# Performance work log

Hardware: AMD Instinct MI355X
Metric: run time of the kernel (lower is better)

Reference implementation:

```python
import jax, jax.numpy as jnp
import numpy as np

ALPHA = 0.2  # LeakyReLU negative slope
NEG_INF = -9e15


def setup_inputs() -> dict:
    key = jax.random.key(0)
    k1, k2, k3, k4, k5 = jax.random.split(key, 5)
    B, N, D = 4, 4096, 256
    feat = jax.random.normal(k1, (B, N, D), dtype=jnp.float32)
    adj = jax.random.randint(k2, (B, N, N), 0, 2, dtype=jnp.int32)
    W = jax.random.normal(k3, (D, D), dtype=jnp.float32) * (1.414 / np.sqrt(D))
    a_1 = jax.random.normal(k4, (D, 1), dtype=jnp.float32) * 0.1
    a_2 = jax.random.normal(k5, (D, 1), dtype=jnp.float32) * 0.1
    return {"feat": feat, "adj": adj, "W": W, "a_1": a_1, "a_2": a_2}


def reference(feat, adj, W, a_1, a_2):
    # h: [B, N, D]
    h = jnp.matmul(feat, W)
    Ax = jnp.matmul(h, a_1)  # [B, N, 1]
    Ay = jnp.matmul(h, a_2)  # [B, N, 1]
    # logits[b, i, j] = Ax[b, j] + Ay[b, i]
    logits = jnp.swapaxes(Ax, 1, 2) + Ay  # [B, N, N]
    e = jax.nn.leaky_relu(logits, negative_slope=ALPHA)
    e = jnp.where(adj > 0, e, jnp.float32(NEG_INF))
    attention = jax.nn.softmax(e, axis=-1)  # dropout p=0.0 -> identity
    h_prime = jnp.matmul(attention, feat)  # [B, N, in_features]
    h_out = jnp.matmul(h_prime, W)  # [B, N, out_features]
    return jax.nn.elu(h_out)
```

## Files before the change

kernel.cpp:

```cpp
#include <hip/hip_runtime.h>

typedef __attribute__((ext_vector_type(8))) short short8;
typedef __attribute__((ext_vector_type(4))) float f32x4;
typedef __attribute__((ext_vector_type(4))) int i32x4;
typedef __attribute__((ext_vector_type(2))) unsigned u32x2;

#define LOG2E 1.44269504f

__device__ __forceinline__ short f2bf(float f) {
  unsigned u = __builtin_bit_cast(unsigned, f);
  u += 0x7fffu + ((u >> 16) & 1u);
  return (short)(u >> 16);
}

__global__ __launch_bounds__(256) void gat_pro(
    const float* __restrict__ feat, const float* __restrict__ W,
    const float* __restrict__ a1, const float* __restrict__ a2,
    short* __restrict__ featB, short* __restrict__ WB,
    float* __restrict__ AxL, float* __restrict__ AyL) {
  __shared__ __align__(16) float a1f[256], a2f[256];
  __shared__ __align__(16) float w1f[256], w2f[256];
  __shared__ __align__(16) float tile[32][260];
  const int tid = threadIdx.x;
  const int f = blockIdx.x, b = blockIdx.y;

  a1f[tid] = a1[tid];
  a2f[tid] = a2[tid];
  __syncthreads();

  {
    float s1 = 0.f, s2 = 0.f;
    const float4* wr = (const float4*)(W + (size_t)tid * 256);
    for (int d0 = 0; d0 < 64; ++d0) {
      float4 v = wr[d0];
      s1 += v.x * a1f[d0 * 4] + v.y * a1f[d0 * 4 + 1] + v.z * a1f[d0 * 4 + 2] + v.w * a1f[d0 * 4 + 3];
      s2 += v.x * a2f[d0 * 4] + v.y * a2f[d0 * 4 + 1] + v.z * a2f[d0 * 4 + 2] + v.w * a2f[d0 * 4 + 3];
    }
    w1f[tid] = s1;
    w2f[tid] = s2;
  }
  __syncthreads();

  {
    const int r = tid >> 3, g8 = tid & 7;
    const float* frow = feat + ((size_t)(b * 4096 + f * 32 + r)) * 256;
    float s1 = 0.f, s2 = 0.f;
#pragma unroll
    for (int k = 0; k < 8; ++k) {
      const int c4 = g8 + 8 * k;
      float4 v = *(const float4*)(frow + c4 * 4);
      float4 u1 = *(const float4*)&w1f[c4 * 4];
      float4 u2 = *(const float4*)&w2f[c4 * 4];
      s1 += v.x * u1.x + v.y * u1.y + v.z * u1.z + v.w * u1.w;
      s2 += v.x * u2.x + v.y * u2.y + v.z * u2.z + v.w * u2.w;
      *(float4*)&tile[r][c4 * 4] = v;
    }
#pragma unroll
    for (int off = 4; off >= 1; off >>= 1) {
      s1 += __shfl_xor(s1, off);
      s2 += __shfl_xor(s2, off);
    }
    if (g8 == 0) {
      AxL[b * 4096 + f * 32 + r] = s1 * LOG2E;
      AyL[b * 4096 + f * 32 + r] = s2 * LOG2E;
    }
  }
  __syncthreads();

  {
    const int g = tid >> 4, l15 = tid & 15;
    short* d = featB + (((size_t)((b * 128 + f) * 16 + g)) * 64) * 8;
#pragma unroll
    for (int q = 0; q < 4; ++q) {
      short8 v;
#pragma unroll
      for (int j8 = 0; j8 < 8; ++j8) v[j8] = f2bf(tile[q * 8 + j8][g * 16 + l15]);
      *(short8*)(d + (q * 16 + l15) * 8) = v;
    }
  }

  if (b == 0 && f < 8) {
    const int g = tid >> 4, l15 = tid & 15;
    const float* s = W + ((size_t)f * 32) * 256 + g * 16 + l15;
    short* d = WB + (((size_t)(f * 16 + g)) * 64) * 8;
#pragma unroll
    for (int q = 0; q < 4; ++q) {
      short8 v;
#pragma unroll
      for (int j8 = 0; j8 < 8; ++j8) v[j8] = f2bf(s[(q * 8 + j8) * 256]);
      *(short8*)(d + (q * 16 + l15) * 8) = v;
    }
  }
}

__global__ __launch_bounds__(512, 2) void gat_attn(
    const short* __restrict__ featB,
    const int* __restrict__ adj,
    const float* __restrict__ AxL, const float* __restrict__ AyL,
    const short* __restrict__ WB,
    float* __restrict__ out)
{
  __shared__ short smem[33792];
  __shared__ float mred[8];

  const int tid = threadIdx.x;
  const int blk = blockIdx.x;
  const int x = blk & 7;
  const int b = x >> 1;
  const int it = ((blk >> 3) << 1) | (x & 1);
  const int i0 = it << 6;
  const int scoff = (blk >> 3) & 15;

  const int lane = tid & 63;
  const int aw = tid >> 6;

  const float* axb = AxL + b * 4096;
  float mx = -3.4e38f;
  for (int i = tid; i < 4096; i += 512) mx = fmaxf(mx, axb[i]);
#pragma unroll
  for (int off = 32; off >= 1; off >>= 1) mx = fmaxf(mx, __shfl_xor(mx, off));
  if (lane == 0) mred[aw] = mx;
  __syncthreads();
  const float MbLb = fmaxf(fmaxf(fmaxf(mred[0], mred[1]), fmaxf(mred[2], mred[3])),
                           fmaxf(fmaxf(mred[4], mred[5]), fmaxf(mred[6], mred[7])));

  float aLk[8], ddk[8];
#pragma unroll
  for (int k = 0; k < 8; ++k) {
    float ayL = AyL[b * 4096 + i0 + aw * 8 + k];
    float sL = ayL + MbLb;
    float mrL = fmaxf(sL, 0.2f * sL);
    aLk[k] = ayL - mrL;
    ddk[k] = -0.8f * mrL;
  }
  const int* adjr = adj + ((size_t)(b * 4096 + i0 + aw * 8)) * 4096 + lane * 4;
  const float4* axp = (const float4*)(AxL + b * 4096) + lane;

  const int rowg = (aw & 1) << 4;
  const int cgrp = (aw >> 1) << 2;
  const int l15 = lane & 15;
  const int q = lane >> 4;

  f32x4 acc[2][4], lac[2];
#pragma unroll
  for (int r = 0; r < 2; ++r) {
    lac[r] = (f32x4){0.f, 0.f, 0.f, 0.f};
#pragma unroll
    for (int j = 0; j < 4; ++j) acc[r][j] = (f32x4){0.f, 0.f, 0.f, 0.f};
  }

  short8 ones;
#pragma unroll
  for (int j = 0; j < 8; ++j) ones[j] = (short)0x3F80;

  const short* fbb = featB + (size_t)b * 128 * 16 * 64 * 8 + lane * 8;

  i32x4 adv[8];
  float4 axv;
  {
    const int w0 = scoff;
    axv = axp[w0 * 64];
#pragma unroll
    for (int k = 0; k < 8; ++k)
      adv[k] = __builtin_nontemporal_load((const i32x4*)(adjr) + (size_t)k * 1024 + w0 * 64);
  }

  for (int sc = 0; sc < 16; ++sc) {
    const int wsc = (scoff + sc) & 15;
    const int pb = (sc & 1) * 16896;
    {
      const float* af = (const float*)&axv;
#pragma unroll
      for (int k = 0; k < 8; ++k) {
        unsigned pr[4];
#pragma unroll
        for (int u = 0; u < 4; ++u) {
          float v = af[u] + aLk[k];
          float uu = fmaxf(v, fmaf(0.2f, v, ddk[k]));
          unsigned ub = adv[k][u] > 0 ? __builtin_bit_cast(unsigned, uu) : 0xFF800000u;
          float p = __builtin_amdgcn_exp2f(__builtin_bit_cast(float, ub));
          pr[u] = __builtin_bit_cast(unsigned, p) + 0x8000u;
        }
        u32x2 pw;
        pw[0] = __builtin_amdgcn_perm(pr[1], pr[0], 0x07060302u);
        pw[1] = __builtin_amdgcn_perm(pr[3], pr[2], 0x07060302u);
        *(u32x2*)(smem + pb + (aw * 8 + k) * 264 + lane * 4) = pw;
      }
    }
    __syncthreads();

    if (sc < 15) {
      const int wn = (scoff + sc + 1) & 15;
      axv = axp[wn * 64];
#pragma unroll
      for (int k = 0; k < 8; ++k)
        adv[k] = __builtin_nontemporal_load((const i32x4*)(adjr) + (size_t)k * 1024 + wn * 64);
    }

#pragma unroll
    for (int h = 0; h < 8; ++h) {
      const int f = wsc * 8 + h;
      const short* fb = fbb + (((size_t)f * 16 + cgrp) << 9);
      short8 a0 = *(const short8*)(smem + pb + (rowg + l15) * 264 + h * 32 + q * 8);
      short8 a1 = *(const short8*)(smem + pb + (rowg + 32 + l15) * 264 + h * 32 + q * 8);
      lac[0] = __builtin_amdgcn_mfma_f32_16x16x32_bf16(a0, ones, lac[0], 0, 0, 0);
      lac[1] = __builtin_amdgcn_mfma_f32_16x16x32_bf16(a1, ones, lac[1], 0, 0, 0);
#pragma unroll
      for (int ct = 0; ct < 4; ++ct) {
        short8 bf = *(const short8*)(fb + (ct << 9));
        acc[0][ct] = __builtin_amdgcn_mfma_f32_16x16x32_bf16(a0, bf, acc[0][ct], 0, 0, 0);
        acc[1][ct] = __builtin_amdgcn_mfma_f32_16x16x32_bf16(a1, bf, acc[1][ct], 0, 0, 0);
      }
    }
  }

  float linv[2][4];
#pragma unroll
  for (int r = 0; r < 2; ++r)
#pragma unroll
    for (int reg = 0; reg < 4; ++reg) {
      float l = lac[r][reg];
      linv[r][reg] = l > 0.f ? 1.f / l : 0.f;
    }

  __syncthreads();
  short* hbuf = smem;
#pragma unroll
  for (int r = 0; r < 2; ++r)
#pragma unroll
    for (int reg = 0; reg < 4; ++reg) {
      const int lr = rowg + r * 32 + q * 4 + reg;
#pragma unroll
      for (int ct = 0; ct < 4; ++ct)
        hbuf[lr * 264 + cgrp * 16 + ct * 16 + l15] = f2bf(acc[r][ct][reg] * linv[r][reg]);
    }
  __syncthreads();

  f32x4 ac2[2][4];
#pragma unroll
  for (int r = 0; r < 2; ++r)
#pragma unroll
    for (int j = 0; j < 4; ++j) ac2[r][j] = (f32x4){0.f, 0.f, 0.f, 0.f};

  const short* wbb = WB + lane * 8;
#pragma unroll
  for (int f = 0; f < 8; ++f) {
    short8 a0 = *(const short8*)&hbuf[(rowg + l15) * 264 + f * 32 + q * 8];
    short8 a1 = *(const short8*)&hbuf[(rowg + 32 + l15) * 264 + f * 32 + q * 8];
    const short* wb = wbb + (((size_t)f * 16 + cgrp) << 9);
#pragma unroll
    for (int ct = 0; ct < 4; ++ct) {
      short8 bf = *(const short8*)(wb + (ct << 9));
      ac2[0][ct] = __builtin_amdgcn_mfma_f32_16x16x32_bf16(a0, bf, ac2[0][ct], 0, 0, 0);
      ac2[1][ct] = __builtin_amdgcn_mfma_f32_16x16x32_bf16(a1, bf, ac2[1][ct], 0, 0, 0);
    }
  }

#pragma unroll
  for (int r = 0; r < 2; ++r)
#pragma unroll
    for (int reg = 0; reg < 4; ++reg) {
      const int row = i0 + rowg + r * 32 + q * 4 + reg;
      float* orow = out + ((size_t)(b * 4096 + row)) * 256 + cgrp * 16 + l15;
#pragma unroll
      for (int ct = 0; ct < 4; ++ct) {
        float v = ac2[r][ct][reg];
        float o = v > 0.f ? v : (__builtin_amdgcn_exp2f(v * LOG2E) - 1.f);
        __builtin_nontemporal_store(o, orow + ct * 16);
      }
    }
}

extern "C" void kernel_launch(void* const* d_in, const int* in_sizes, int n_in,
                              void* d_out, int out_size, void* d_ws, size_t ws_size,
                              hipStream_t stream) {
  (void)in_sizes; (void)n_in; (void)out_size; (void)ws_size;
  const float* feat = (const float*)d_in[0];
  const int* adj = (const int*)d_in[1];
  const float* W = (const float*)d_in[2];
  const float* a1 = (const float*)d_in[3];
  const float* a2 = (const float*)d_in[4];
  float* out = (float*)d_out;

  char* ws = (char*)d_ws;
  short* featB   = (short*)ws;
  short* WB      = (short*)(ws + 8388608);
  float* AxL     = (float*)(ws + 8519680);
  float* AyL     = (float*)(ws + 8585216);

  hipLaunchKernelGGL(gat_pro, dim3(128, 4), dim3(256), 0, stream, feat, W, a1, a2, featB, WB, AxL, AyL);
  hipLaunchKernelGGL(gat_attn, dim3(256), dim3(512), 0, stream, featB, adj, AxL, AyL, WB, out);
}
```

Measured before the change: 429.1 us.

## Split main loop into producer and consumer waves for warp specialization

Splits the 8 waves into 4 producer waves and 4 consumer waves. Producers load adjacency, compute the masked exponentials and write bf16 probabilities into a double-buffered shared tile one chunk ahead. Consumers run all the MFMA work on 64 rows by 64 columns each. The aim is to overlap the exp/VALU work and global loads with the matrix multiplies. The cost is a higher per-wave register load (16 adjacency vectors, or 16 accumulators) and only half the waves issuing MFMA, so occupancy or MFMA throughput may suffer.

```diff
diff --git a/kernel.cpp b/kernel.cpp
--- a/kernel.cpp
+++ b/kernel.cpp
@@ -113,6 +113,8 @@
 
   const int lane = tid & 63;
   const int aw = tid >> 6;
+  const int l15 = lane & 15;
+  const int q = lane >> 4;
 
   const float* axb = AxL + b * 4096;
   float mx = -3.4e38f;
@@ -124,117 +126,129 @@
   const float MbLb = fmaxf(fmaxf(fmaxf(mred[0], mred[1]), fmaxf(mred[2], mred[3])),
                            fmaxf(fmaxf(mred[4], mred[5]), fmaxf(mred[6], mred[7])));
 
-  float aLk[8], ddk[8];
-#pragma unroll
-  for (int k = 0; k < 8; ++k) {
-    float ayL = AyL[b * 4096 + i0 + aw * 8 + k];
-    float sL = ayL + MbLb;
-    float mrL = fmaxf(sL, 0.2f * sL);
-    aLk[k] = ayL - mrL;
-    ddk[k] = -0.8f * mrL;
-  }
-  const int* adjr = adj + ((size_t)(b * 4096 + i0 + aw * 8)) * 4096 + lane * 4;
+  const bool producer = (aw < 4);
+
+  const int pw = aw & 3;
+  float aLk[16], ddk[16];
+  const int* adjr = adj + ((size_t)(b * 4096 + i0 + pw * 16)) * 4096 + lane * 4;
   const float4* axp = (const float4*)(AxL + b * 4096) + lane;
+  i32x4 adv[16];
+  float4 axv;
+
+  const int cg = (aw & 3) << 2;
+  const short* fbb = featB + (size_t)b * 128 * 16 * 64 * 8 + lane * 8;
+  f32x4 acc[4][4], lac[4];
+#pragma unroll
+  for (int r = 0; r < 4; ++r) {
+    lac[r] = (f32x4){0.f, 0.f, 0.f, 0.f};
+#pragma unroll
+    for (int j = 0; j < 4; ++j) acc[r][j] = (f32x4){0.f, 0.f, 0.f, 0.f};
+  }
+  short8 ones;
+#pragma unroll
+  for (int j = 0; j < 8; ++j) ones[j] = (short)0x3F80;
+
+  if (producer) {
+#pragma unroll
+    for (int k = 0; k < 16; ++k) {
+      float ayL = AyL[b * 4096 + i0 + pw * 16 + k];
+      float sL = ayL + MbLb;
+      float mrL = fmaxf(sL, 0.2f * sL);
+      aLk[k] = ayL - mrL;
+      ddk[k] = -0.8f * mrL;
+    }
+  }
+
+  auto computeP = [&](int bufSel) {
+    const float* af = (const float*)&axv;
+#pragma unroll
+    for (int k = 0; k < 16; ++k) {
+      unsigned pr[4];
+#pragma unroll
+      for (int u = 0; u < 4; ++u) {
+        float v = af[u] + aLk[k];
+        float uu = fmaxf(v, fmaf(0.2f, v, ddk[k]));
+        unsigned ub = adv[k][u] > 0 ? __builtin_bit_cast(unsigned, uu) : 0xFF800000u;
+        float p = __builtin_amdgcn_exp2f(__builtin_bit_cast(float, ub));
+        pr[u] = __builtin_bit_cast(unsigned, p) + 0x8000u;
+      }
+      u32x2 pw2;
+      pw2[0] = __builtin_amdgcn_perm(pr[1], pr[0], 0x07060302u);
+      pw2[1] = __builtin_amdgcn_perm(pr[3], pr[2], 0x07060302u);
+      *(u32x2*)(smem + bufSel * 16896 + (pw * 16 + k) * 264 + lane * 4) = pw2;
+    }
+  };
+  auto prefetchW = [&](int w) {
+    axv = axp[w * 64];
+#pragma unroll
+    for (int k = 0; k < 16; ++k)
+      adv[k] = __builtin_nontemporal_load((const i32x4*)(adjr) + (size_t)k * 1024 + w * 64);
+  };
+
+  if (producer) {
+    prefetchW(scoff);
+    computeP(0);
+    prefetchW((scoff + 1) & 15);
+  }
+  __syncthreads();
+
+  for (int sc = 0; sc < 16; ++sc) {
+    if (producer) {
+      if (sc < 15) {
+        computeP((sc + 1) & 1);
+        if (sc < 14) prefetchW((scoff + sc + 2) & 15);
+      }
+    } else {
+      const int wsc = (scoff + sc) & 15;
+      const int pb = (sc & 1) * 16896;
+#pragma unroll
+      for (int h = 0; h < 8; ++h) {
+        const int f = wsc * 8 + h;
+        const short* fb = fbb + (((size_t)f * 16 + cg) << 9);
+        short8 a[4];
+#pragma unroll
+        for (int r = 0; r < 4; ++r)
+          a[r] = *(const short8*)(smem + pb + (r * 16 + l15) * 264 + h * 32 + q * 8);
+#pragma unroll
+        for (int r = 0; r < 4; ++r)
+          lac[r] = __builtin_amdgcn_mfma_f32_16x16x32_bf16(a[r], ones, lac[r], 0, 0, 0);
+#pragma unroll
+        for (int ct = 0; ct < 4; ++ct) {
+          short8 bf = *(const short8*)(fb + (ct << 9));
+#pragma unroll
+          for (int r = 0; r < 4; ++r)
+            acc[r][ct] = __builtin_amdgcn_mfma_f32_16x16x32_bf16(a[r], bf, acc[r][ct], 0, 0, 0);
+        }
+      }
+    }
+    __syncthreads();
+  }
+
+  if (!producer) {
+    float linv[4][4];
+#pragma unroll
+    for (int r = 0; r < 4; ++r)
+#pragma unroll
+      for (int reg = 0; reg < 4; ++reg) {
+        float l = lac[r][reg];
+        linv[r][reg] = l > 0.f ? 1.f / l : 0.f;
+      }
+    short* hbuf = smem;
+#pragma unroll
+    for (int r = 0; r < 4; ++r)
+#pragma unroll
+      for (int reg = 0; reg < 4; ++reg) {
+        const int lr = r * 16 + q * 4 + reg;
+#pragma unroll
+        for (int ct = 0; ct < 4; ++ct)
+          hbuf[lr * 264 + (cg + ct) * 16 + l15] = f2bf(acc[r][ct][reg] * linv[r][reg]);
+      }
+  }
+  __syncthreads();
 
   const int rowg = (aw & 1) << 4;
   const int cgrp = (aw >> 1) << 2;
-  const int l15 = lane & 15;
-  const int q = lane >> 4;
-
-  f32x4 acc[2][4], lac[2];
-#pragma unroll
-  for (int r = 0; r < 2; ++r) {
-    lac[r] = (f32x4){0.f, 0.f, 0.f, 0.f};
-#pragma unroll
-    for (int j = 0; j < 4; ++j) acc[r][j] = (f32x4){0.f, 0.f, 0.f, 0.f};
-  }
-
-  short8 ones;
-#pragma unroll
-  for (int j = 0; j < 8; ++j) ones[j] = (short)0x3F80;
-
-  const short* fbb = featB + (size_t)b * 128 * 16 * 64 * 8 + lane * 8;
-
-  i32x4 adv[8];
-  float4 axv;
-  {
-    const int w0 = scoff;
-    axv = axp[w0 * 64];
-#pragma unroll
-    for (int k = 0; k < 8; ++k)
-      adv[k] = __builtin_nontemporal_load((const i32x4*)(adjr) + (size_t)k * 1024 + w0 * 64);
-  }
-
-  for (int sc = 0; sc < 16; ++sc) {
-    const int wsc = (scoff + sc) & 15;
-    const int pb = (sc & 1) * 16896;
-    {
-      const float* af = (const float*)&axv;
-#pragma unroll
-      for (int k = 0; k < 8; ++k) {
-        unsigned pr[4];
-#pragma unroll
-        for (int u = 0; u < 4; ++u) {
-          float v = af[u] + aLk[k];
-          float uu = fmaxf(v, fmaf(0.2f, v, ddk[k]));
-          unsigned ub = adv[k][u] > 0 ? __builtin_bit_cast(unsigned, uu) : 0xFF800000u;
-          float p = __builtin_amdgcn_exp2f(__builtin_bit_cast(float, ub));
-          pr[u] = __builtin_bit_cast(unsigned, p) + 0x8000u;
-        }
-        u32x2 pw;
-        pw[0] = __builtin_amdgcn_perm(pr[1], pr[0], 0x07060302u);
-        pw[1] = __builtin_amdgcn_perm(pr[3], pr[2], 0x07060302u);
-        *(u32x2*)(smem + pb + (aw * 8 + k) * 264 + lane * 4) = pw;
-      }
-    }
-    __syncthreads();
-
-    if (sc < 15) {
-      const int wn = (scoff + sc + 1) & 15;
-      axv = axp[wn * 64];
-#pragma unroll
-      for (int k = 0; k < 8; ++k)
-        adv[k] = __builtin_nontemporal_load((const i32x4*)(adjr) + (size_t)k * 1024 + wn * 64);
-    }
-
-#pragma unroll
-    for (int h = 0; h < 8; ++h) {
-      const int f = wsc * 8 + h;
-      const short* fb = fbb + (((size_t)f * 16 + cgrp) << 9);
-      short8 a0 = *(const short8*)(smem + pb + (rowg + l15) * 264 + h * 32 + q * 8);
-      short8 a1 = *(const short8*)(smem + pb + (rowg + 32 + l15) * 264 + h * 32 + q * 8);
-      lac[0] = __builtin_amdgcn_mfma_f32_16x16x32_bf16(a0, ones, lac[0], 0, 0, 0);
-      lac[1] = __builtin_amdgcn_mfma_f32_16x16x32_bf16(a1, ones, lac[1], 0, 0, 0);
-#pragma unroll
-      for (int ct = 0; ct < 4; ++ct) {
-        short8 bf = *(const short8*)(fb + (ct << 9));
-        acc[0][ct] = __builtin_amdgcn_mfma_f32_16x16x32_bf16(a0, bf, acc[0][ct], 0, 0, 0);
-        acc[1][ct] = __builtin_amdgcn_mfma_f32_16x16x32_bf16(a1, bf, acc[1][ct], 0, 0, 0);
-      }
-    }
-  }
-
-  float linv[2][4];
-#pragma unroll
-  for (int r = 0; r < 2; ++r)
-#pragma unroll
-    for (int reg = 0; reg < 4; ++reg) {
-      float l = lac[r][reg];
-      linv[r][reg] = l > 0.f ? 1.f / l : 0.f;
-    }
-
-  __syncthreads();
   short* hbuf = smem;
-#pragma unroll
-  for (int r = 0; r < 2; ++r)
-#pragma unroll
-    for (int reg = 0; reg < 4; ++reg) {
-      const int lr = rowg + r * 32 + q * 4 + reg;
-#pragma unroll
-      for (int ct = 0; ct < 4; ++ct)
-        hbuf[lr * 264 + cgrp * 16 + ct * 16 + l15] = f2bf(acc[r][ct][reg] * linv[r][reg]);
-    }
-  __syncthreads();
 
   f32x4 ac2[2][4];
 #pragma unroll
```

Result: slower. 441.7 us (+2.9%).

## Pack adjacency into bitmasks in prologue kernel and read bits in attention

Applied to the files above, without the earlier changes.

Adds a second z-slice to the prologue kernel that reads the int32 adjacency matrix and packs it into 64-bit ballot bitmasks in workspace. The attention kernel then loads one 64-bit word per row chunk instead of int32 vectors and tests bits to apply the mask. This shrinks adjacency traffic in the MFMA-heavy attention kernel, but the full 256 MB adjacency read still happens, now in the prologue, plus an extra small write and read. Overall bytes do not drop, so any benefit depends on moving that read out of the compute-overlapped loop.

```diff
diff --git a/kernel.cpp b/kernel.cpp
--- a/kernel.cpp
+++ b/kernel.cpp
@@ -2,8 +2,8 @@
 
 typedef __attribute__((ext_vector_type(8))) short short8;
 typedef __attribute__((ext_vector_type(4))) float f32x4;
-typedef __attribute__((ext_vector_type(4))) int i32x4;
 typedef __attribute__((ext_vector_type(2))) unsigned u32x2;
+typedef __attribute__((ext_vector_type(4))) unsigned long long ull4;
 
 #define LOG2E 1.44269504f
 
@@ -16,13 +16,38 @@
 __global__ __launch_bounds__(256) void gat_pro(
     const float* __restrict__ feat, const float* __restrict__ W,
     const float* __restrict__ a1, const float* __restrict__ a2,
+    const int* __restrict__ adj,
     short* __restrict__ featB, short* __restrict__ WB,
-    float* __restrict__ AxL, float* __restrict__ AyL) {
+    float* __restrict__ AxL, float* __restrict__ AyL,
+    unsigned long long* __restrict__ adjP) {
+  const int tid = threadIdx.x;
+  const int f = blockIdx.x, b = blockIdx.y;
+
+  if (blockIdx.z == 1) {
+    const int wv = tid >> 6, l = tid & 63;
+#pragma unroll 1
+    for (int r = 0; r < 8; ++r) {
+      const int row = f * 32 + wv * 8 + r;
+      const int* src = adj + ((size_t)(b * 4096 + row)) * 4096;
+      unsigned long long* dst = adjP + ((size_t)(b * 4096 + row)) * 64;
+#pragma unroll 4
+      for (int jc = 0; jc < 16; ++jc) {
+        unsigned long long m0 = __ballot(src[jc * 256 + 0 * 64 + l] > 0);
+        unsigned long long m1 = __ballot(src[jc * 256 + 1 * 64 + l] > 0);
+        unsigned long long m2 = __ballot(src[jc * 256 + 2 * 64 + l] > 0);
+        unsigned long long m3 = __ballot(src[jc * 256 + 3 * 64 + l] > 0);
+        if (l == 0) {
+          ull4 mv = (ull4){m0, m1, m2, m3};
+          *(ull4*)(dst + jc * 4) = mv;
+        }
+      }
+    }
+    return;
+  }
+
   __shared__ __align__(16) float a1f[256], a2f[256];
   __shared__ __align__(16) float w1f[256], w2f[256];
   __shared__ __align__(16) float tile[32][260];
-  const int tid = threadIdx.x;
-  const int f = blockIdx.x, b = blockIdx.y;
 
   a1f[tid] = a1[tid];
   a2f[tid] = a2[tid];
@@ -95,7 +120,7 @@
 
 __global__ __launch_bounds__(512, 2) void gat_attn(
     const short* __restrict__ featB,
-    const int* __restrict__ adj,
+    const unsigned long long* __restrict__ adjP,
     const float* __restrict__ AxL, const float* __restrict__ AyL,
     const short* __restrict__ WB,
     float* __restrict__ out)
@@ -133,8 +158,10 @@
     aLk[k] = ayL - mrL;
     ddk[k] = -0.8f * mrL;
   }
-  const int* adjr = adj + ((size_t)(b * 4096 + i0 + aw * 8)) * 4096 + lane * 4;
+  const unsigned long long* adjPr =
+      adjP + ((size_t)(b * 4096 + i0 + aw * 8)) * 64 + (lane >> 4);
   const float4* axp = (const float4*)(AxL + b * 4096) + lane;
+  const int sh = (lane & 15) * 4;
 
   const int rowg = (aw & 1) << 4;
   const int cgrp = (aw >> 1) << 2;
@@ -155,14 +182,13 @@
 
   const short* fbb = featB + (size_t)b * 128 * 16 * 64 * 8 + lane * 8;
 
-  i32x4 adv[8];
+  unsigned long long adv[8];
   float4 axv;
   {
     const int w0 = scoff;
     axv = axp[w0 * 64];
 #pragma unroll
-    for (int k = 0; k < 8; ++k)
-      adv[k] = __builtin_nontemporal_load((const i32x4*)(adjr) + (size_t)k * 1024 + w0 * 64);
+    for (int k = 0; k < 8; ++k) adv[k] = adjPr[(size_t)k * 64 + w0 * 4];
   }
 
   for (int sc = 0; sc < 16; ++sc) {
@@ -177,7 +203,8 @@
         for (int u = 0; u < 4; ++u) {
           float v = af[u] + aLk[k];
           float uu = fmaxf(v, fmaf(0.2f, v, ddk[k]));
-          unsigned ub = adv[k][u] > 0 ? __builtin_bit_cast(unsigned, uu) : 0xFF800000u;
+          unsigned ub = ((adv[k] >> (sh + u)) & 1ull)
+                            ? __builtin_bit_cast(unsigned, uu) : 0xFF800000u;
           float p = __builtin_amdgcn_exp2f(__builtin_bit_cast(float, ub));
           pr[u] = __builtin_bit_cast(unsigned, p) + 0x8000u;
         }
@@ -193,8 +220,7 @@
       const int wn = (scoff + sc + 1) & 15;
       axv = axp[wn * 64];
 #pragma unroll
-      for (int k = 0; k < 8; ++k)
-        adv[k] = __builtin_nontemporal_load((const i32x4*)(adjr) + (size_t)k * 1024 + wn * 64);
+      for (int k = 0; k < 8; ++k) adv[k] = adjPr[(size_t)k * 64 + wn * 4];
     }
 
 #pragma unroll
@@ -283,11 +309,14 @@
   float* out = (float*)d_out;
 
   char* ws = (char*)d_ws;
-  short* featB   = (short*)ws;
-  short* WB      = (short*)(ws + 8388608);
-  float* AxL     = (float*)(ws + 8519680);
-  float* AyL     = (float*)(ws + 8585216);
-
-  hipLaunchKernelGGL(gat_pro, dim3(128, 4), dim3(256), 0, stream, feat, W, a1, a2, featB, WB, AxL, AyL);
-  hipLaunchKernelGGL(gat_attn, dim3(256), dim3(512), 0, stream, featB, adj, AxL, AyL, WB, out);
+  short* featB = (short*)ws;
+  short* WB    = (short*)(ws + 8388608);
+  float* AxL   = (float*)(ws + 8519680);
+  float* AyL   = (float*)(ws + 8585216);
+  unsigned long long* adjP = (unsigned long long*)(ws + 8650752);
+
+  hipLaunchKernelGGL(gat_pro, dim3(128, 4, 2), dim3(256), 0, stream,
+                     feat, W, a1, a2, adj, featB, WB, AxL, AyL, adjP);
+  hipLaunchKernelGGL(gat_attn, dim3(256), dim3(512), 0, stream,
+                     featB, adjP, AxL, AyL, WB, out);
 }
```

Result: slower. 506.4 us (+18.0%).
